# Optimization experiments

Hardware: AMD Instinct MI355X
Metric: run time of the kernel (lower is better)

The kernel has to match this reference:

```python
import jax, jax.numpy as jnp
import numpy as np

N_LEAVES = 32768
DEPTH = 16               # tree levels, leaves at level 0
N_NODES = 2 * N_LEAVES - 1
H = 256                  # h_size
X = 300                  # x_size
FEAT = 1024              # image feature_size
R = 49                   # image regions
VOCAB = 30000
CLASSES = 5


def setup_inputs() -> dict:
    ks = jax.random.split(jax.random.key(0), 10)
    wordid = jax.random.randint(ks[0], (N_NODES,), 0, VOCAB, dtype=jnp.int32)
    # leaves carry word tokens (mask=1), internal nodes don't (mask=0)
    mask = jnp.concatenate([jnp.ones(N_LEAVES, jnp.int32),
                            jnp.zeros(N_NODES - N_LEAVES, jnp.int32)])
    image = jax.random.normal(ks[1], (R, FEAT), dtype=jnp.float32)
    h0 = jnp.zeros((N_NODES, H), jnp.float32)
    c0 = jnp.zeros((N_NODES, H), jnp.float32)
    s = lambda k, shp, fan: jax.random.normal(k, shp, dtype=jnp.float32) * (1.0 / np.sqrt(fan))
    emb = s(ks[2], (VOCAB, X), X)
    attn_w_in = s(ks[3], (X, FEAT), FEAT)            # Attention.linear_in (no bias)
    attn_w_out = s(ks[4], (X, X + FEAT), X + FEAT)   # Attention.linear_out
    attn_b_out = jnp.zeros((X,), jnp.float32)
    w_iou = s(ks[5], (3 * H, X), X)                  # cell.W_iou (no bias)
    u_iou = s(ks[6], (3 * H, 2 * H), 2 * H)          # cell.U_iou (no bias)
    b_iou = jnp.zeros((1, 3 * H), jnp.float32)
    u_f_w = s(ks[7], (2 * H, 2 * H), 2 * H)          # cell.U_f
    u_f_b = jnp.zeros((2 * H,), jnp.float32)
    lin_w = s(ks[8], (CLASSES, H), H)                # final classifier
    lin_b = jnp.zeros((CLASSES,), jnp.float32)
    return dict(wordid=wordid, mask=mask, image=image, h0=h0, c0=c0, emb=emb,
                attn_w_in=attn_w_in, attn_w_out=attn_w_out, attn_b_out=attn_b_out,
                w_iou=w_iou, u_iou=u_iou, b_iou=b_iou, u_f_w=u_f_w, u_f_b=u_f_b,
                lin_w=lin_w, lin_b=lin_b)


def _forward(wordid, mask, image, h0, c0, emb, attn_w_in, attn_w_out, attn_b_out,
             w_iou, u_iou, b_iou, u_f_w, u_f_b, lin_w, lin_b):
    # --- embedding + attention over image regions ---
    embeds = emb[wordid * mask]                                  # [N, X]
    img_in = image @ attn_w_in.T                                 # [R, X]
    atten = jax.nn.softmax(embeds @ img_in.T, axis=1)            # [N, R]
    context = atten @ image                                      # [N, FEAT]
    sent = jnp.tanh(jnp.concatenate([context, embeds], axis=1) @ attn_w_out.T + attn_b_out)
    iou_x = (sent @ w_iou.T) * mask[:, None].astype(sent.dtype)  # [N, 3H] (dropout p=0 -> identity)

    def apply_node(iou, c_in):
        i, o, u = jnp.split(iou + b_iou, 3, axis=1)
        c_new = jax.nn.sigmoid(i) * jnp.tanh(u) + c_in
        return jax.nn.sigmoid(o) * jnp.tanh(c_new), c_new

    # --- leaves: no mailbox, apply_node with initial c ---
    h_leaf, c_leaf = apply_node(iou_x[:N_LEAVES], c0[:N_LEAVES])
    h = h0.at[:N_LEAVES].set(h_leaf)
    c = c0.at[:N_LEAVES].set(c_leaf)

    # --- topological propagation, one dense level at a time ---
    off_prev, sz, off = 0, N_LEAVES, N_LEAVES
    for _ in range(DEPTH - 1):
        sz_new = sz // 2
        h_cat = jax.lax.dynamic_slice_in_dim(h, off_prev, sz).reshape(sz_new, 2 * H)
        c_ch = jax.lax.dynamic_slice_in_dim(c, off_prev, sz).reshape(sz_new, 2, H)
        f = jax.nn.sigmoid(h_cat @ u_f_w.T + u_f_b).reshape(sz_new, 2, H)
        c_red = jnp.sum(f * c_ch, axis=1)                        # [sz_new, H]
        iou = h_cat @ u_iou.T                                    # reduce_func overwrites node iou
        h_new, c_new = apply_node(iou, c_red)
        h = h.at[off:off + sz_new].set(h_new)
        c = c.at[off:off + sz_new].set(c_new)
        off_prev, sz, off = off, sz_new, off + sz_new

    return h @ lin_w.T + lin_b                                   # [N, CLASSES]


def reference(wordid, mask, image, h0, c0, emb, attn_w_in, attn_w_out, attn_b_out,
              w_iou, u_iou, b_iou, u_f_w, u_f_b, lin_w, lin_b):
    return _forward(wordid, mask, image, h0, c0, emb, attn_w_in, attn_w_out, attn_b_out,
                    w_iou, u_iou, b_iou, u_f_w, u_f_b, lin_w, lin_b)
```

## Files before the change

kernel.cpp:

```cpp
#include <hip/hip_runtime.h>
#include <hip/hip_bf16.h>
#include <math.h>

#define N_LEAVES 32768
#define N_NODES  65535
#define DEPTH    16
#define H        256
#define XS       300
#define FEAT     1024
#define RR       49
#define CLASSES  5

#define XP 320
#define CATW 384

typedef __attribute__((ext_vector_type(8))) short bf16x8;
typedef __attribute__((ext_vector_type(4))) float f32x4;

__device__ __forceinline__ ushort f2bf(float v) {
    __hip_bfloat16 h = __float2bfloat16(v);
    return *reinterpret_cast<ushort*>(&h);
}
__device__ __forceinline__ float bf2f(ushort u) {
    __hip_bfloat16 h; *reinterpret_cast<ushort*>(&h) = u;
    return __bfloat162float(h);
}

__device__ __forceinline__ float fsig(float x) {
    float e = __builtin_amdgcn_exp2f(-1.44269504f * x);
    return __builtin_amdgcn_rcpf(1.0f + e);
}
__device__ __forceinline__ float ftanh(float x) {
    float xx = fmaxf(x, -20.0f);
    float e = __builtin_amdgcn_exp2f(-2.88539008f * xx);
    return (1.0f - e) * __builtin_amdgcn_rcpf(1.0f + e);
}
__device__ __forceinline__ float fexp(float x) {
    return __builtin_amdgcn_exp2f(1.44269504f * x);
}

#define SPIN() __builtin_amdgcn_sched_barrier(0)
#define SBAR() { __builtin_amdgcn_s_barrier(); __builtin_amdgcn_sched_barrier(0); }

__device__ __forceinline__ void swz_mj(int& mblk, int& jg) {
    int lid = blockIdx.y * gridDim.x + blockIdx.x;
    int mcount = gridDim.y, njg = gridDim.x;
    if ((mcount & 7) == 0) {
        int xcd = lid & 7, q = lid >> 3;
        jg = q % njg;
        mblk = xcd * (mcount >> 3) + q / njg;
    } else { mblk = blockIdx.y; jg = blockIdx.x; }
}

__device__ __forceinline__ ushort* lds_at(ushort* base, int row, int kbyte) {
    int off = row * 128 + kbyte;
    off ^= ((row & 7) << 4);
    return (ushort*)((char*)base + off);
}

__device__ __forceinline__ void gll16(const void* g, void* l) {
    __builtin_amdgcn_global_load_lds(
        (const __attribute__((address_space(1))) unsigned int*)g,
        (__attribute__((address_space(3))) unsigned int*)l, 16, 0, 0);
}

__device__ __forceinline__ void issue_tileA(const ushort* A, long lda, long m0, long mmax,
                                            int k0, ushort* buf, int R, int w, int lane)
{
    const int insts = R >> 5;
#pragma unroll
    for (int q = 0; q < 4; ++q) {
        if (q >= insts) break;
        int dest = (w * insts + q) * 1024;
        int row = (dest >> 7) + (lane >> 3);
        int kb = ((lane & 7) << 4) ^ ((row & 7) << 4);
        long am = m0 + row; if (am > mmax) am = mmax;
        gll16((const char*)(A + am * lda + k0) + kb, (char*)buf + dest);
    }
}

__global__ __launch_bounds__(256)
void k_sent(const ushort* __restrict__ A, const ushort* __restrict__ Wf,
            const float* __restrict__ bias, ushort* __restrict__ Cbf)
{
    __shared__ ushort At[3][128 * 64];
    const int tid = threadIdx.x;
    const int l = tid & 63;
    const int w = tid >> 6;
    int mblk, nb; swz_mj(mblk, nb);
    const long m0 = (long)mblk * 128;
    const ushort* wb = Wf + (size_t)(nb * 4 + w) * 24 * 512 + l * 8;

    bf16x8 wreg[2][2][2];
    f32x4 acc[2][8] = {};

    auto loadW = [&](int t, int buf) {
        const ushort* wt = wb + (long)t * 4 * 512;
#pragma unroll
        for (int kk = 0; kk < 2; ++kk)
#pragma unroll
            for (int j = 0; j < 2; ++j)
                wreg[buf][kk][j] = *(const bf16x8*)(wt + (long)(kk * 2 + j) * 512);
    };

    issue_tileA(A, CATW, m0, N_LEAVES - 1, 0, At[0], 128, w, l);
    __syncthreads();
    issue_tileA(A, CATW, m0, N_LEAVES - 1, 64, At[1], 128, w, l);
    SPIN();
    loadW(0, 0);
#pragma unroll
    for (int t = 0; t < 6; ++t) {
        if (t + 2 < 6) issue_tileA(A, CATW, m0, N_LEAVES - 1, (t + 2) * 64, At[(t + 2) % 3], 128, w, l);
        SPIN();
        if (t + 1 < 6) loadW(t + 1, (t + 1) & 1);
        ushort* Ab = At[t % 3];
#pragma unroll
        for (int kk = 0; kk < 2; ++kk) {
            bf16x8 af[8];
#pragma unroll
            for (int i = 0; i < 8; ++i)
                af[i] = *(const bf16x8*)lds_at(Ab, i * 16 + (l & 15), kk * 64 + (l >> 4) * 16);
#pragma unroll
            for (int j = 0; j < 2; ++j)
#pragma unroll
                for (int i = 0; i < 8; ++i)
                    acc[j][i] = __builtin_amdgcn_mfma_f32_16x16x32_bf16(af[i], wreg[t & 1][kk][j], acc[j][i], 0, 0, 0);
        }
        if (t + 1 < 6) SBAR();
    }
#pragma unroll
    for (int j = 0; j < 2; ++j) {
        long n = (long)nb * 128 + w * 32 + j * 16 + (l & 15);
        if (n >= XS) continue;
        float bn = bias[n];
#pragma unroll
        for (int i = 0; i < 8; ++i)
#pragma unroll
            for (int r = 0; r < 4; ++r) {
                long m = m0 + i * 16 + (l >> 4) * 4 + r;
                Cbf[m * XP + n] = f2bf(ftanh(acc[j][i][r] + bn));
            }
    }
}

__global__ __launch_bounds__(256)
void k_attn(const float* __restrict__ emb, const int* __restrict__ wid,
            const ushort* __restrict__ img, ushort* __restrict__ cat)
{
    __shared__ ushort At[128 * 64];
    __shared__ ushort Bt[64 * 64];
    const int tid = threadIdx.x;
    const int l = tid & 63;
    const int w = tid >> 6;
    const long m0 = (long)blockIdx.x * 128;
    const int srow = tid >> 3, skg = tid & 7;

    int wrd[4];
#pragma unroll
    for (int q = 0; q < 4; ++q) wrd[q] = wid[m0 + q * 32 + srow];

    float av[4][8];
    bf16x8 breg[2];
    f32x4 acc[2][4] = {};

    auto loadAB = [&](int t) {
        int c = t * 64 + skg * 8;
#pragma unroll
        for (int q = 0; q < 4; ++q) {
            const float* er = emb + (long)wrd[q] * XS;
            if (c + 8 <= XS) {
                float4 a = *(const float4*)(er + c);
                float4 b = *(const float4*)(er + c + 4);
                av[q][0] = a.x; av[q][1] = a.y; av[q][2] = a.z; av[q][3] = a.w;
                av[q][4] = b.x; av[q][5] = b.y; av[q][6] = b.z; av[q][7] = b.w;
            } else {
#pragma unroll
                for (int u = 0; u < 8; ++u) av[q][u] = (c + u < XS) ? er[c + u] : 0.f;
            }
        }
#pragma unroll
        for (int q = 0; q < 2; ++q)
            breg[q] = *(const bf16x8*)(img + (long)(q * 32 + srow) * XP + t * 64 + skg * 8);
    };
    auto writeAB = [&](int t) {
        int c = t * 64 + skg * 8;
#pragma unroll
        for (int q = 0; q < 4; ++q) {
            int row = q * 32 + srow;
            bf16x8 pk;
#pragma unroll
            for (int u = 0; u < 8; ++u) pk[u] = (short)f2bf(av[q][u]);
            *(bf16x8*)lds_at(At, row, skg * 16) = pk;
            *(bf16x8*)(cat + (m0 + row) * CATW + 64 + c) = pk;
        }
#pragma unroll
        for (int q = 0; q < 2; ++q)
            *(bf16x8*)lds_at(Bt, q * 32 + srow, skg * 16) = breg[q];
    };

    loadAB(0);
    writeAB(0);
    for (int t = 0; t < 5; ++t) {
        __syncthreads();
        if (t + 1 < 5) loadAB(t + 1);
#pragma unroll
        for (int kk = 0; kk < 2; ++kk) {
            bf16x8 af[2], bg[4];
#pragma unroll
            for (int i = 0; i < 2; ++i)
                af[i] = *(const bf16x8*)lds_at(At, w * 32 + i * 16 + (l & 15), kk * 64 + (l >> 4) * 16);
#pragma unroll
            for (int j = 0; j < 4; ++j)
                bg[j] = *(const bf16x8*)lds_at(Bt, j * 16 + (l & 15), kk * 64 + (l >> 4) * 16);
#pragma unroll
            for (int i = 0; i < 2; ++i)
#pragma unroll
                for (int j = 0; j < 4; ++j)
                    acc[i][j] = __builtin_amdgcn_mfma_f32_16x16x32_bf16(af[i], bg[j], acc[i][j], 0, 0, 0);
        }
        if (t + 1 < 5) {
            __syncthreads();
            writeAB(t + 1);
        }
    }
#pragma unroll
    for (int i = 0; i < 2; ++i)
#pragma unroll
        for (int r = 0; r < 4; ++r) {
            long m = m0 + w * 32 + i * 16 + (l >> 4) * 4 + r;
            float v[4]; float mx = -1e30f;
#pragma unroll
            for (int j = 0; j < 4; ++j) {
                int n = j * 16 + (l & 15);
                v[j] = (n < RR) ? acc[i][j][r] : -1e30f;
                mx = fmaxf(mx, v[j]);
            }
#pragma unroll
            for (int sh = 1; sh < 16; sh <<= 1) mx = fmaxf(mx, __shfl_xor(mx, sh));
            float e[4], s = 0.f;
#pragma unroll
            for (int j = 0; j < 4; ++j) { e[j] = fexp(v[j] - mx); s += e[j]; }
#pragma unroll
            for (int sh = 1; sh < 16; sh <<= 1) s += __shfl_xor(s, sh);
            float inv = __builtin_amdgcn_rcpf(s);
#pragma unroll
            for (int j = 0; j < 4; ++j)
                cat[m * CATW + j * 16 + (l & 15)] = f2bf(e[j] * inv);
        }
}

__global__ __launch_bounds__(256)
void k_leaf_fused(const ushort* __restrict__ A, const ushort* __restrict__ Wf,
                  const float* __restrict__ b_iou,
                  ushort* __restrict__ h, ushort* __restrict__ c)
{
    __shared__ ushort At[3][128 * 64];
    const int tid = threadIdx.x;
    const int l = tid & 63;
    const int w = tid >> 6;
    int mblk, jg; swz_mj(mblk, jg);
    const long m0 = (long)mblk * 128;
    const ushort* wb = Wf + (size_t)(jg * 4 + w) * 30 * 512 + l * 8;

    bf16x8 wreg[2][2][3];
    f32x4 acc[3][8] = {};

    auto loadW = [&](int t, int buf) {
        const ushort* wt = wb + (long)t * 6 * 512;
#pragma unroll
        for (int kk = 0; kk < 2; ++kk)
#pragma unroll
            for (int g = 0; g < 3; ++g)
                wreg[buf][kk][g] = *(const bf16x8*)(wt + (long)(kk * 3 + g) * 512);
    };

    issue_tileA(A, XP, m0, N_LEAVES - 1, 0, At[0], 128, w, l);
    __syncthreads();
    issue_tileA(A, XP, m0, N_LEAVES - 1, 64, At[1], 128, w, l);
    SPIN();
    loadW(0, 0);
#pragma unroll
    for (int t = 0; t < 5; ++t) {
        if (t + 2 < 5) issue_tileA(A, XP, m0, N_LEAVES - 1, (t + 2) * 64, At[(t + 2) % 3], 128, w, l);
        SPIN();
        if (t + 1 < 5) loadW(t + 1, (t + 1) & 1);
        ushort* Ab = At[t % 3];
#pragma unroll
        for (int kk = 0; kk < 2; ++kk) {
            bf16x8 af[8];
#pragma unroll
            for (int i = 0; i < 8; ++i)
                af[i] = *(const bf16x8*)lds_at(Ab, i * 16 + (l & 15), kk * 64 + (l >> 4) * 16);
#pragma unroll
            for (int g = 0; g < 3; ++g)
#pragma unroll
                for (int i = 0; i < 8; ++i)
                    acc[g][i] = __builtin_amdgcn_mfma_f32_16x16x32_bf16(af[i], wreg[t & 1][kk][g], acc[g][i], 0, 0, 0);
        }
        if (t + 1 < 5) SBAR();
    }
    {
        int jglob = jg * 64 + w * 16 + (l & 15);
        float bi = b_iou[jglob], bu = b_iou[512 + jglob], bo = b_iou[256 + jglob];
#pragma unroll
        for (int i = 0; i < 8; ++i)
#pragma unroll
            for (int r = 0; r < 4; ++r) {
                long m = m0 + i * 16 + (l >> 4) * 4 + r;
                float cn = fsig(acc[0][i][r] + bi) * ftanh(acc[1][i][r] + bu);
                c[m * H + jglob] = f2bf(cn);
                h[m * H + jglob] = f2bf(fsig(acc[2][i][r] + bo) * ftanh(cn));
            }
    }
}

__global__ __launch_bounds__(256)
void k_tree_fused(const ushort* __restrict__ A, const ushort* __restrict__ Wf,
                  const float* __restrict__ u_f_b, const float* __restrict__ b_iou,
                  const ushort* __restrict__ csrc,
                  ushort* __restrict__ hdst, ushort* __restrict__ cdst, int sz_new)
{
    __shared__ ushort At[4][64 * 64];
    const int tid = threadIdx.x;
    const int l = tid & 63;
    const int w = tid >> 6;
    int mblk, jg; swz_mj(mblk, jg);
    const long m0 = (long)mblk * 64;
    const ushort* wb = Wf + (size_t)(jg * 4 + w) * 80 * 512 + l * 8;

    bf16x8 wreg[2][2][5];
    f32x4 acc[5][4] = {};

    auto loadW = [&](int t, int buf) {
        const ushort* wt = wb + (long)t * 10 * 512;
#pragma unroll
        for (int kk = 0; kk < 2; ++kk)
#pragma unroll
            for (int g = 0; g < 5; ++g)
                wreg[buf][kk][g] = *(const bf16x8*)(wt + (long)(kk * 5 + g) * 512);
    };

    issue_tileA(A, 512, m0, sz_new - 1, 0, At[0], 64, w, l);
    __syncthreads();
    issue_tileA(A, 512, m0, sz_new - 1, 64, At[1], 64, w, l);
    SPIN();
    loadW(0, 0);
    SPIN();
    issue_tileA(A, 512, m0, sz_new - 1, 128, At[2], 64, w, l);
#pragma unroll
    for (int t = 0; t < 8; ++t) {
        if (t + 1 < 8) loadW(t + 1, (t + 1) & 1);
        SPIN();
        if (t + 3 < 8) issue_tileA(A, 512, m0, sz_new - 1, (t + 3) * 64, At[(t + 3) & 3], 64, w, l);
        SPIN();
        ushort* Ab = At[t & 3];
#pragma unroll
        for (int kk = 0; kk < 2; ++kk) {
            bf16x8 af[4];
#pragma unroll
            for (int i = 0; i < 4; ++i)
                af[i] = *(const bf16x8*)lds_at(Ab, i * 16 + (l & 15), kk * 64 + (l >> 4) * 16);
#pragma unroll
            for (int g = 0; g < 5; ++g)
#pragma unroll
                for (int i = 0; i < 4; ++i)
                    acc[g][i] = __builtin_amdgcn_mfma_f32_16x16x32_bf16(af[i], wreg[t & 1][kk][g], acc[g][i], 0, 0, 0);
        }
        if (t + 1 < 8) SBAR();
    }
    {
        int jglob = jg * 64 + w * 16 + (l & 15);
        float bf0 = u_f_b[jglob], bf1 = u_f_b[256 + jglob];
        float bi = b_iou[jglob], bu = b_iou[512 + jglob], bo = b_iou[256 + jglob];
#pragma unroll
        for (int i = 0; i < 4; ++i)
#pragma unroll
            for (int r = 0; r < 4; ++r) {
                long m = m0 + i * 16 + (l >> 4) * 4 + r;
                if (m < sz_new) {
                    float cl = bf2f(csrc[(2 * m) * H + jglob]);
                    float cr = bf2f(csrc[(2 * m + 1) * H + jglob]);
                    float S = fsig(acc[0][i][r] + bf0) * cl
                            + fsig(acc[1][i][r] + bf1) * cr;
                    float cn = fsig(acc[2][i][r] + bi) * ftanh(acc[3][i][r] + bu) + S;
                    cdst[m * H + jglob] = f2bf(cn);
                    hdst[m * H + jglob] = f2bf(fsig(acc[4][i][r] + bo) * ftanh(cn));
                }
            }
    }
}

#define PREP_NB   7350
#define CVT_NB    352
#define W3F_NB    960
#define W5F_NB    2560

__global__ __launch_bounds__(256)
void k_prep_a(const float* __restrict__ image, const float* __restrict__ w_in,
              const float* __restrict__ w_out, const float* __restrict__ w_iou,
              const float* __restrict__ u_f_w, const float* __restrict__ u_iou,
              ushort* __restrict__ img_bf, ushort* __restrict__ wcat,
              ushort* __restrict__ w3f, ushort* __restrict__ w5f)
{
    int b = blockIdx.x;
    if (b < PREP_NB) {
        const int wave = (b * 256 + threadIdx.x) >> 6;
        const int lane = threadIdx.x & 63;
        const int half = RR * XS;
        if (wave >= 2 * half) return;
        const float* wr; const float* ir; ushort* outp;
        if (wave < half) {
            int r = wave / XS, x = wave % XS;
            ir = image + (long)r * FEAT;
            wr = w_in + (long)x * FEAT;
            outp = img_bf + (long)r * XP + x;
        } else {
            int w2 = wave - half;
            int x = w2 / RR, r = w2 % RR;
            ir = image + (long)r * FEAT;
            wr = w_out + (long)x * (FEAT + XS);
            outp = wcat + (long)x * CATW + r;
        }
        float s = 0.f;
#pragma unroll
        for (int u = 0; u < FEAT / 64; ++u) {
            int f = lane + u * 64;
            s = fmaf(ir[f], wr[f], s);
        }
#pragma unroll
        for (int sh = 32; sh; sh >>= 1) s += __shfl_xor(s, sh);
        if (lane == 0) *outp = f2bf(s);
    } else if (b < PREP_NB + CVT_NB) {
        long idx = (long)(b - PREP_NB) * 256 + threadIdx.x;
        if (idx >= (long)XS * XS) return;
        int r = (int)(idx / XS), cc = (int)(idx % XS);
        wcat[(long)r * CATW + 64 + cc] = f2bf(w_out[(long)r * (FEAT + XS) + FEAT + cc]);
    } else if (b < PREP_NB + CVT_NB + W3F_NB) {
        long idx = (long)(b - PREP_NB - CVT_NB) * 256 + threadIdx.x;
        if (idx >= 245760) return;
        int u = idx & 7; long r = idx >> 3;
        int l = r & 63; r >>= 6;
        int g = (int)(r % 3); r /= 3;
        int kk = r & 1; r >>= 1;
        int t = (int)(r % 5); r /= 5;
        int wq = r & 3; r >>= 2;
        int jg = (int)r;
        int row = jg * 64 + wq * 16 + (l & 15);
        int col = t * 64 + kk * 32 + (l >> 4) * 8 + u;
        int srow = (g == 0) ? row : (g == 1) ? 512 + row : 256 + row;
        w3f[idx] = (col < XS) ? f2bf(w_iou[(long)srow * XS + col]) : 0;
    } else {
        long idx = (long)(b - PREP_NB - CVT_NB - W3F_NB) * 256 + threadIdx.x;
        if (idx >= 655360) return;
        int u = idx & 7; long r = idx >> 3;
        int l = r & 63; r >>= 6;
        int g = (int)(r % 5); r /= 5;
        int kk = r & 1; r >>= 1;
        int t = (int)(r & 7); r >>= 3;
        int wq = r & 3; r >>= 2;
        int jg = (int)r;
        int row = jg * 64 + wq * 16 + (l & 15);
        int col = t * 64 + kk * 32 + (l >> 4) * 8 + u;
        const float* src;
        if (g == 0)      src = u_f_w + (long)row * 512;
        else if (g == 1) src = u_f_w + (long)(256 + row) * 512;
        else if (g == 2) src = u_iou + (long)row * 512;
        else if (g == 3) src = u_iou + (long)(512 + row) * 512;
        else             src = u_iou + (long)(256 + row) * 512;
        w5f[idx] = f2bf(src[col]);
    }
}

__global__ __launch_bounds__(256)
void k_prep_b(ushort* __restrict__ dst, const ushort* __restrict__ wcat)
{
    long idx = (long)blockIdx.x * 256 + threadIdx.x;
    if (idx >= 147456) return;
    int u = idx & 7; long r = idx >> 3;
    int l = r & 63; r >>= 6;
    int j = r & 1; r >>= 1;
    int kk = r & 1; r >>= 1;
    int t = (int)(r % 6); r /= 6;
    int wq = r & 3; r >>= 2;
    int nb = (int)r;
    int row = nb * 128 + wq * 32 + j * 16 + (l & 15);
    int col = t * 64 + kk * 32 + (l >> 4) * 8 + u;
    dst[idx] = wcat[(long)row * CATW + col];
}

__global__ __launch_bounds__(256)
void k_classify(const ushort* __restrict__ h, const float* __restrict__ lin_w,
                const float* __restrict__ lin_b, float* __restrict__ out, int n_rows)
{
    const int node = (int)((blockIdx.x * 256 + threadIdx.x) >> 6);
    const int lane = threadIdx.x & 63;
    if (node >= n_rows) return;
    ushort4 hv4 = *(const ushort4*)(h + (long)node * H + lane * 4);
    float hv[4] = { bf2f(hv4.x), bf2f(hv4.y), bf2f(hv4.z), bf2f(hv4.w) };
    float p[CLASSES];
#pragma unroll
    for (int cc = 0; cc < CLASSES; ++cc) {
        float4 wv = *(const float4*)(lin_w + (long)cc * H + lane * 4);
        p[cc] = hv[0] * wv.x + hv[1] * wv.y + hv[2] * wv.z + hv[3] * wv.w;
    }
#pragma unroll
    for (int cc = 0; cc < CLASSES; ++cc)
#pragma unroll
        for (int sh = 32; sh; sh >>= 1) p[cc] += __shfl_xor(p[cc], sh);
    if (lane == 0) {
#pragma unroll
        for (int cc = 0; cc < CLASSES; ++cc)
            out[(long)node * CLASSES + cc] = p[cc] + lin_b[cc];
    }
}

extern "C" void kernel_launch(void* const* d_in, const int* in_sizes, int n_in,
                              void* d_out, int out_size, void* d_ws, size_t ws_size,
                              hipStream_t stream)
{
    const int*   wordid     = (const int*)  d_in[0];
    const float* image      = (const float*)d_in[2];
    const float* emb        = (const float*)d_in[5];
    const float* attn_w_in  = (const float*)d_in[6];
    const float* attn_w_out = (const float*)d_in[7];
    const float* attn_b_out = (const float*)d_in[8];
    const float* w_iou      = (const float*)d_in[9];
    const float* u_iou      = (const float*)d_in[10];
    const float* b_iou      = (const float*)d_in[11];
    const float* u_f_w      = (const float*)d_in[12];
    const float* u_f_b      = (const float*)d_in[13];
    const float* lin_w      = (const float*)d_in[14];
    const float* lin_b      = (const float*)d_in[15];
    float* out = (float*)d_out;

    char* p = (char*)d_ws;
    auto alloc = [&](size_t bytes) { char* r = p; p += (bytes + 255) & ~255UL; return r; };
    ushort* cat     = (ushort*)alloc((size_t)N_LEAVES * CATW * 2);
    ushort* sentbf  = (ushort*)alloc((size_t)N_LEAVES * XP * 2);
    ushort* hall    = (ushort*)alloc((size_t)65536 * H * 2);
    ushort* cA      = (ushort*)alloc((size_t)N_LEAVES * H * 2);
    ushort* cB      = (ushort*)alloc((size_t)(N_LEAVES/2) * H * 2);
    ushort* img_bf  = (ushort*)alloc((size_t)64 * XP * 2);
    ushort* wcat    = (ushort*)alloc((size_t)CATW * CATW * 2);
    ushort* wcatf   = (ushort*)alloc((size_t)147456 * 2);
    ushort* w3f     = (ushort*)alloc((size_t)245760 * 2);
    ushort* w5f     = (ushort*)alloc((size_t)655360 * 2);
    (void)ws_size;

    hipMemsetAsync(img_bf, 0, (size_t)64 * XP * 2, stream);
    hipMemsetAsync(wcat,   0, (size_t)CATW * CATW * 2, stream);
    k_prep_a<<<PREP_NB + CVT_NB + W3F_NB + W5F_NB, 256, 0, stream>>>(
        image, attn_w_in, attn_w_out, w_iou, u_f_w, u_iou,
        img_bf, wcat, w3f, w5f);
    k_prep_b<<<(147456 + 255) / 256, 256, 0, stream>>>(wcatf, wcat);

    k_attn<<<N_LEAVES / 128, 256, 0, stream>>>(emb, wordid, img_bf, cat);
    k_sent<<<dim3(3, N_LEAVES / 128), 256, 0, stream>>>(cat, wcatf, attn_b_out, sentbf);
    k_leaf_fused<<<dim3(4, N_LEAVES / 128), 256, 0, stream>>>(
        sentbf, w3f, b_iou, hall, cA);

    ushort* csrc = cA; ushort* cdst = cB;
    int node_off = N_LEAVES;
    int sz = N_LEAVES;
    int off_prev = 0;
    for (int lvl = 0; lvl < DEPTH - 1; ++lvl) {
        int sz_new = sz / 2;
        k_tree_fused<<<dim3(4, (sz_new + 63) / 64), 256, 0, stream>>>(
            hall + (long)off_prev * H, w5f, u_f_b, b_iou, csrc,
            hall + (long)node_off * H, cdst, sz_new);
        off_prev = node_off;
        node_off += sz_new;
        ushort* t = csrc; csrc = cdst; cdst = t;
        sz = sz_new;
    }

    k_classify<<<((long)N_NODES * 64 + 255) / 256, 256, 0, stream>>>(
        hall, lin_w, lin_b, out, N_NODES);
}
```

Measured before the change: 311.6 us.

## Restructure attention kernel with prefragmented image weights and raise MFMA wave priority

Measured after the change: 326.6 us. 1.05x slower.

```diff
diff --git a/kernel.cpp b/kernel.cpp
--- a/kernel.cpp
+++ b/kernel.cpp
@@ -41,6 +41,8 @@
 
 #define SPIN() __builtin_amdgcn_sched_barrier(0)
 #define SBAR() { __builtin_amdgcn_s_barrier(); __builtin_amdgcn_sched_barrier(0); }
+#define PRIO1() __builtin_amdgcn_s_setprio(1)
+#define PRIO0() __builtin_amdgcn_s_setprio(0)
 
 __device__ __forceinline__ void swz_mj(int& mblk, int& jg) {
     int lid = blockIdx.y * gridDim.x + blockIdx.x;
@@ -114,6 +116,7 @@
         SPIN();
         if (t + 1 < 6) loadW(t + 1, (t + 1) & 1);
         ushort* Ab = At[t % 3];
+        PRIO1();
 #pragma unroll
         for (int kk = 0; kk < 2; ++kk) {
             bf16x8 af[8];
@@ -126,6 +129,7 @@
                 for (int i = 0; i < 8; ++i)
                     acc[j][i] = __builtin_amdgcn_mfma_f32_16x16x32_bf16(af[i], wreg[t & 1][kk][j], acc[j][i], 0, 0, 0);
         }
+        PRIO0();
         if (t + 1 < 6) SBAR();
     }
 #pragma unroll
@@ -145,94 +149,64 @@
 
 __global__ __launch_bounds__(256)
 void k_attn(const float* __restrict__ emb, const int* __restrict__ wid,
-            const ushort* __restrict__ img, ushort* __restrict__ cat)
-{
-    __shared__ ushort At[128 * 64];
-    __shared__ ushort Bt[64 * 64];
+            const ushort* __restrict__ imgf, ushort* __restrict__ cat)
+{
+    __shared__ ushort E[5][64 * 64];
     const int tid = threadIdx.x;
     const int l = tid & 63;
     const int w = tid >> 6;
-    const long m0 = (long)blockIdx.x * 128;
-    const int srow = tid >> 3, skg = tid & 7;
-
-    int wrd[4];
-#pragma unroll
-    for (int q = 0; q < 4; ++q) wrd[q] = wid[m0 + q * 32 + srow];
-
-    float av[4][8];
-    bf16x8 breg[2];
-    f32x4 acc[2][4] = {};
-
-    auto loadAB = [&](int t) {
-        int c = t * 64 + skg * 8;
-#pragma unroll
-        for (int q = 0; q < 4; ++q) {
-            const float* er = emb + (long)wrd[q] * XS;
-            if (c + 8 <= XS) {
-                float4 a = *(const float4*)(er + c);
-                float4 b = *(const float4*)(er + c + 4);
-                av[q][0] = a.x; av[q][1] = a.y; av[q][2] = a.z; av[q][3] = a.w;
-                av[q][4] = b.x; av[q][5] = b.y; av[q][6] = b.z; av[q][7] = b.w;
+    const long m0 = (long)blockIdx.x * 64;
+
+    {
+        int row = tid >> 2;
+        int q = tid & 3;
+        const float* er = emb + (long)wid[m0 + row] * XS;
+#pragma unroll
+        for (int u = 0; u < 10; ++u) {
+            int ccol = q * 80 + u * 8;
+            bf16x8 pk;
+            if (ccol + 8 <= XS) {
+                float4 a = *(const float4*)(er + ccol);
+                float4 b = *(const float4*)(er + ccol + 4);
+                pk[0] = (short)f2bf(a.x); pk[1] = (short)f2bf(a.y);
+                pk[2] = (short)f2bf(a.z); pk[3] = (short)f2bf(a.w);
+                pk[4] = (short)f2bf(b.x); pk[5] = (short)f2bf(b.y);
+                pk[6] = (short)f2bf(b.z); pk[7] = (short)f2bf(b.w);
             } else {
 #pragma unroll
-                for (int u = 0; u < 8; ++u) av[q][u] = (c + u < XS) ? er[c + u] : 0.f;
+                for (int e = 0; e < 8; ++e)
+                    pk[e] = (ccol + e < XS) ? (short)f2bf(er[ccol + e]) : (short)0;
             }
-        }
-#pragma unroll
-        for (int q = 0; q < 2; ++q)
-            breg[q] = *(const bf16x8*)(img + (long)(q * 32 + srow) * XP + t * 64 + skg * 8);
-    };
-    auto writeAB = [&](int t) {
-        int c = t * 64 + skg * 8;
-#pragma unroll
-        for (int q = 0; q < 4; ++q) {
-            int row = q * 32 + srow;
-            bf16x8 pk;
-#pragma unroll
-            for (int u = 0; u < 8; ++u) pk[u] = (short)f2bf(av[q][u]);
-            *(bf16x8*)lds_at(At, row, skg * 16) = pk;
-            *(bf16x8*)(cat + (m0 + row) * CATW + 64 + c) = pk;
-        }
-#pragma unroll
-        for (int q = 0; q < 2; ++q)
-            *(bf16x8*)lds_at(Bt, q * 32 + srow, skg * 16) = breg[q];
-    };
-
-    loadAB(0);
-    writeAB(0);
-    for (int t = 0; t < 5; ++t) {
-        __syncthreads();
-        if (t + 1 < 5) loadAB(t + 1);
-#pragma unroll
-        for (int kk = 0; kk < 2; ++kk) {
-            bf16x8 af[2], bg[4];
-#pragma unroll
-            for (int i = 0; i < 2; ++i)
-                af[i] = *(const bf16x8*)lds_at(At, w * 32 + i * 16 + (l & 15), kk * 64 + (l >> 4) * 16);
-#pragma unroll
-            for (int j = 0; j < 4; ++j)
-                bg[j] = *(const bf16x8*)lds_at(Bt, j * 16 + (l & 15), kk * 64 + (l >> 4) * 16);
-#pragma unroll
-            for (int i = 0; i < 2; ++i)
-#pragma unroll
-                for (int j = 0; j < 4; ++j)
-                    acc[i][j] = __builtin_amdgcn_mfma_f32_16x16x32_bf16(af[i], bg[j], acc[i][j], 0, 0, 0);
-        }
-        if (t + 1 < 5) {
-            __syncthreads();
-            writeAB(t + 1);
-        }
-    }
-#pragma unroll
-    for (int i = 0; i < 2; ++i)
+            *(bf16x8*)lds_at(E[ccol >> 6], row, (ccol & 63) * 2) = pk;
+            *(bf16x8*)(cat + (m0 + row) * CATW + 64 + ccol) = pk;
+        }
+    }
+    __syncthreads();
+
+    {
+        f32x4 sacc[4] = {};
+        const ushort* ib = imgf + l * 8;
+        PRIO1();
+#pragma unroll
+        for (int t = 0; t < 5; ++t)
+#pragma unroll
+            for (int kk = 0; kk < 2; ++kk) {
+                bf16x8 af = *(const bf16x8*)lds_at(E[t], w * 16 + (l & 15), kk * 64 + (l >> 4) * 16);
+#pragma unroll
+                for (int j = 0; j < 4; ++j) {
+                    bf16x8 bg = *(const bf16x8*)(ib + (long)((j * 5 + t) * 2 + kk) * 512);
+                    sacc[j] = __builtin_amdgcn_mfma_f32_16x16x32_bf16(af, bg, sacc[j], 0, 0, 0);
+                }
+            }
+        PRIO0();
 #pragma unroll
         for (int r = 0; r < 4; ++r) {
-            long m = m0 + w * 32 + i * 16 + (l >> 4) * 4 + r;
+            int row = w * 16 + (l >> 4) * 4 + r;
             float v[4]; float mx = -1e30f;
 #pragma unroll
             for (int j = 0; j < 4; ++j) {
                 int n = j * 16 + (l & 15);
-                v[j] = (n < RR) ? acc[i][j][r] : -1e30f;
+                v[j] = (n < RR) ? sacc[j][r] : -1e30f;
                 mx = fmaxf(mx, v[j]);
             }
 #pragma unroll
@@ -245,8 +219,9 @@
             float inv = __builtin_amdgcn_rcpf(s);
 #pragma unroll
             for (int j = 0; j < 4; ++j)
-                cat[m * CATW + j * 16 + (l & 15)] = f2bf(e[j] * inv);
-        }
+                cat[(m0 + row) * CATW + j * 16 + (l & 15)] = f2bf(e[j] * inv);
+        }
+    }
 }
 
 __global__ __launch_bounds__(256)
@@ -285,6 +260,7 @@
         SPIN();
         if (t + 1 < 5) loadW(t + 1, (t + 1) & 1);
         ushort* Ab = At[t % 3];
+        PRIO1();
 #pragma unroll
         for (int kk = 0; kk < 2; ++kk) {
             bf16x8 af[8];
@@ -297,6 +273,7 @@
                 for (int i = 0; i < 8; ++i)
                     acc[g][i] = __builtin_amdgcn_mfma_f32_16x16x32_bf16(af[i], wreg[t & 1][kk][g], acc[g][i], 0, 0, 0);
         }
+        PRIO0();
         if (t + 1 < 5) SBAR();
     }
     {
@@ -354,6 +331,7 @@
         if (t + 3 < 8) issue_tileA(A, 512, m0, sz_new - 1, (t + 3) * 64, At[(t + 3) & 3], 64, w, l);
         SPIN();
         ushort* Ab = At[t & 3];
+        PRIO1();
 #pragma unroll
         for (int kk = 0; kk < 2; ++kk) {
             bf16x8 af[4];
@@ -366,6 +344,7 @@
                 for (int i = 0; i < 4; ++i)
                     acc[g][i] = __builtin_amdgcn_mfma_f32_16x16x32_bf16(af[i], wreg[t & 1][kk][g], acc[g][i], 0, 0, 0);
         }
+        PRIO0();
         if (t + 1 < 8) SBAR();
     }
     {
@@ -471,21 +450,38 @@
     }
 }
 
-__global__ __launch_bounds__(256)
-void k_prep_b(ushort* __restrict__ dst, const ushort* __restrict__ wcat)
-{
-    long idx = (long)blockIdx.x * 256 + threadIdx.x;
-    if (idx >= 147456) return;
-    int u = idx & 7; long r = idx >> 3;
-    int l = r & 63; r >>= 6;
-    int j = r & 1; r >>= 1;
-    int kk = r & 1; r >>= 1;
-    int t = (int)(r % 6); r /= 6;
-    int wq = r & 3; r >>= 2;
-    int nb = (int)r;
-    int row = nb * 128 + wq * 32 + j * 16 + (l & 15);
-    int col = t * 64 + kk * 32 + (l >> 4) * 8 + u;
-    dst[idx] = wcat[(long)row * CATW + col];
+#define WCATF_NB 576
+#define IMGF_NB  80
+__global__ __launch_bounds__(256)
+void k_prep_b(ushort* __restrict__ wcatf, ushort* __restrict__ imgf,
+              const ushort* __restrict__ wcat, const ushort* __restrict__ img_bf)
+{
+    int b = blockIdx.x;
+    if (b < WCATF_NB) {
+        long idx = (long)b * 256 + threadIdx.x;
+        if (idx >= 147456) return;
+        int u = idx & 7; long r = idx >> 3;
+        int l = r & 63; r >>= 6;
+        int j = r & 1; r >>= 1;
+        int kk = r & 1; r >>= 1;
+        int t = (int)(r % 6); r /= 6;
+        int wq = r & 3; r >>= 2;
+        int nb = (int)r;
+        int row = nb * 128 + wq * 32 + j * 16 + (l & 15);
+        int col = t * 64 + kk * 32 + (l >> 4) * 8 + u;
+        wcatf[idx] = wcat[(long)row * CATW + col];
+    } else {
+        long idx = (long)(b - WCATF_NB) * 256 + threadIdx.x;
+        if (idx >= 20480) return;
+        int u = idx & 7; long r = idx >> 3;
+        int l = r & 63; r >>= 6;
+        int kk = r & 1; r >>= 1;
+        int t = (int)(r % 5); r /= 5;
+        int j = (int)r;
+        int row = j * 16 + (l & 15);
+        int col = t * 64 + kk * 32 + (l >> 4) * 8 + u;
+        imgf[idx] = img_bf[(long)row * XP + col];
+    }
 }
 
 __global__ __launch_bounds__(256)
@@ -542,6 +538,7 @@
     ushort* cB      = (ushort*)alloc((size_t)(N_LEAVES/2) * H * 2);
     ushort* img_bf  = (ushort*)alloc((size_t)64 * XP * 2);
     ushort* wcat    = (ushort*)alloc((size_t)CATW * CATW * 2);
+    ushort* imgf    = (ushort*)alloc((size_t)20480 * 2);
     ushort* wcatf   = (ushort*)alloc((size_t)147456 * 2);
     ushort* w3f     = (ushort*)alloc((size_t)245760 * 2);
     ushort* w5f     = (ushort*)alloc((size_t)655360 * 2);
@@ -552,9 +549,9 @@
     k_prep_a<<<PREP_NB + CVT_NB + W3F_NB + W5F_NB, 256, 0, stream>>>(
         image, attn_w_in, attn_w_out, w_iou, u_f_w, u_iou,
         img_bf, wcat, w3f, w5f);
-    k_prep_b<<<(147456 + 255) / 256, 256, 0, stream>>>(wcatf, wcat);
-
-    k_attn<<<N_LEAVES / 128, 256, 0, stream>>>(emb, wordid, img_bf, cat);
+    k_prep_b<<<WCATF_NB + IMGF_NB, 256, 0, stream>>>(wcatf, imgf, wcat, img_bf);
+
+    k_attn<<<N_LEAVES / 64, 256, 0, stream>>>(emb, wordid, imgf, cat);
     k_sent<<<dim3(3, N_LEAVES / 128), 256, 0, stream>>>(cat, wcatf, attn_b_out, sentbf);
     k_leaf_fused<<<dim3(4, N_LEAVES / 128), 256, 0, stream>>>(
         sentbf, w3f, b_iou, hall, cA);
```

## Fuse last six tree levels into one single-block kernel with LDS-resident state

Applied to the files above, without the earlier changes.

New measurement: 512.9 us. +64.6%, slower.

```diff
diff --git a/kernel.cpp b/kernel.cpp
--- a/kernel.cpp
+++ b/kernel.cpp
@@ -387,6 +387,89 @@
                     hdst[m * H + jglob] = f2bf(fsig(acc[4][i][r] + bo) * ftanh(cn));
                 }
             }
+    }
+}
+
+__global__ __launch_bounds__(256)
+void k_tree_tail(ushort* __restrict__ hall, const ushort* __restrict__ Wf,
+                 const float* __restrict__ u_f_b, const float* __restrict__ b_iou,
+                 ushort* __restrict__ cping, ushort* __restrict__ cpong)
+{
+    __shared__ ushort HA[8][32 * 64];
+    __shared__ ushort HB[8][32 * 64];
+    const int tid = threadIdx.x;
+    const int l = tid & 63;
+    const int w = tid >> 6;
+
+    {
+        const ushort* src = hall + (size_t)65408 * H;
+#pragma unroll
+        for (int u = 0; u < 8; ++u) {
+            long idx = ((long)u * 256 + tid) * 8;
+            int row = (int)(idx >> 9), col = (int)(idx & 511);
+            bf16x8 v = *(const bf16x8*)(src + idx);
+            *(bf16x8*)lds_at(HA[col >> 6], row, (col & 63) * 2) = v;
+        }
+    }
+    __syncthreads();
+
+    ushort (*Hin)[32 * 64] = HA;
+    ushort (*Hout)[32 * 64] = HB;
+    ushort* csrc = cping;
+    ushort* cdst = cpong;
+    int off = 65472;
+
+    for (int lvl = 9; lvl <= 14; ++lvl) {
+        int sz_new = 16384 >> lvl;
+#pragma unroll
+        for (int jf = 0; jf < 4; ++jf) {
+            const ushort* wb = Wf + (size_t)(w * 4 + jf) * 80 * 512 + l * 8;
+            f32x4 acc[5][2] = {};
+            for (int t = 0; t < 8; ++t) {
+                const ushort* wt = wb + (long)t * 10 * 512;
+#pragma unroll
+                for (int kk = 0; kk < 2; ++kk) {
+                    bf16x8 af[2];
+#pragma unroll
+                    for (int i = 0; i < 2; ++i)
+                        af[i] = *(const bf16x8*)lds_at(Hin[t], i * 16 + (l & 15), kk * 64 + (l >> 4) * 16);
+#pragma unroll
+                    for (int g = 0; g < 5; ++g) {
+                        bf16x8 bg = *(const bf16x8*)(wt + (long)(kk * 5 + g) * 512);
+#pragma unroll
+                        for (int i = 0; i < 2; ++i)
+                            acc[g][i] = __builtin_amdgcn_mfma_f32_16x16x32_bf16(af[i], bg, acc[g][i], 0, 0, 0);
+                    }
+                }
+            }
+            int jglob = w * 64 + jf * 16 + (l & 15);
+            float bf0 = u_f_b[jglob], bf1 = u_f_b[256 + jglob];
+            float bi = b_iou[jglob], bu = b_iou[512 + jglob], bo = b_iou[256 + jglob];
+#pragma unroll
+            for (int i = 0; i < 2; ++i)
+#pragma unroll
+                for (int r = 0; r < 4; ++r) {
+                    int m = i * 16 + ((l >> 4) * 4 + r);
+                    if (m < sz_new) {
+                        float cl = bf2f(csrc[(2 * m) * H + jglob]);
+                        float cr = bf2f(csrc[(2 * m + 1) * H + jglob]);
+                        float S = fsig(acc[0][i][r] + bf0) * cl
+                                + fsig(acc[1][i][r] + bf1) * cr;
+                        float cn = fsig(acc[2][i][r] + bi) * ftanh(acc[3][i][r] + bu) + S;
+                        float hv = fsig(acc[4][i][r] + bo) * ftanh(cn);
+                        ushort hb = f2bf(hv);
+                        cdst[m * H + jglob] = f2bf(cn);
+                        hall[(size_t)(off + m) * H + jglob] = hb;
+                        int row = m >> 1;
+                        int col = (m & 1) * 256 + jglob;
+                        *lds_at(Hout[col >> 6], row, (col & 63) * 2) = hb;
+                    }
+                }
+        }
+        __syncthreads();
+        ushort (*tmp)[32 * 64] = Hin; Hin = Hout; Hout = tmp;
+        ushort* tc = csrc; csrc = cdst; cdst = tc;
+        off += sz_new;
     }
 }
 
@@ -563,7 +646,7 @@
     int node_off = N_LEAVES;
     int sz = N_LEAVES;
     int off_prev = 0;
-    for (int lvl = 0; lvl < DEPTH - 1; ++lvl) {
+    for (int lvl = 0; lvl < 9; ++lvl) {
         int sz_new = sz / 2;
         k_tree_fused<<<dim3(4, (sz_new + 63) / 64), 256, 0, stream>>>(
             hall + (long)off_prev * H, w5f, u_f_b, b_iou, csrc,
@@ -573,6 +656,7 @@
         ushort* t = csrc; csrc = cdst; cdst = t;
         sz = sz_new;
     }
+    k_tree_tail<<<1, 256, 0, stream>>>(hall, w5f, u_f_b, b_iou, csrc, cdst);
 
     k_classify<<<((long)N_NODES * 64 + 255) / 256, 256, 0, stream>>>(
         hall, lin_w, lin_b, out, N_NODES);
```
